# Kernel optimization log

Hardware: AMD Instinct MI355X
Metric: run time of the kernel (lower is better)

The kernel has to match this reference:

```python
import jax, jax.numpy as jnp
import numpy as np

F = 128          # gnn_out_features
D = 2 * F        # GNN_Emb width (mu || logvar)
N_SRC, N_DST = 50000, 10000
N_CATE, P = 18, 8
E = 100000
TAU = 1.0        # decay time constant (get_decay_weight assumed exp(-dt/tau))


def setup_inputs() -> dict:
    key = jax.random.key(0)
    ks = jax.random.split(key, 8)
    return {
        "gnn_emb_src": jax.random.normal(ks[0], (N_SRC, D), dtype=jnp.float32),
        "gnn_emb_dst": jax.random.normal(ks[1], (N_DST, D), dtype=jnp.float32),
        "news_pref": jax.random.normal(ks[2], (N_DST, N_CATE, P, D), dtype=jnp.float32),
        "last_update_time": jax.random.uniform(ks[3], (N_DST, N_CATE, P), dtype=jnp.float32),
        "time": jax.random.uniform(ks[4], (E,), dtype=jnp.float32),
        "cate_id": jax.random.randint(ks[5], (N_SRC,), 0, N_CATE),
        "src_idx": jax.random.randint(ks[6], (E,), 0, N_SRC),
        "dst_idx": jax.random.randint(ks[7], (E,), 0, N_DST),
    }


def reference(gnn_emb_src, gnn_emb_dst, news_pref, last_update_time,
              time, cate_id, src_idx, dst_idx):
    # --- per-edge gathers (DGL edges.src / edges.dst) ---
    src_emb = gnn_emb_src[src_idx, :F]                 # Representation, sample<=0  [E, F]
    cate = cate_id[src_idx]                            # [E]
    lut = last_update_time[dst_idx, cate]              # category-specific       [E, P]
    pref = news_pref[dst_idx, cate]                    # category-specific       [E, P, D]

    # --- decay-weighted fusion ---
    delta_t = time[0] - lut                            # Time[0] - Last_Update_Time [E, P]
    w = jnp.exp(-delta_t / TAU)                        # get_decay_weight         [E, P]
    target = gnn_emb_dst[dst_idx][:, None, :]          # dst GNN_Emb broadcast    [E, 1, D]
    decayed = pref * w[..., None] + target * (1.0 - w[..., None])  # [E, P, D]
    pref_emb = decayed[..., :F]                        # mu half, sample<=0       [E, P, F]

    # --- scaled dot-product attention: query=src_emb over P pref slots ---
    scores = jnp.einsum('ef,epf->ep', src_emb, pref_emb) / jnp.sqrt(jnp.float32(F))
    attn = jax.nn.softmax(scores, axis=-1)             # [E, P]
    dst_pref_emb = jnp.einsum('ep,epf->ef', attn, pref_emb)  # [E, F]

    # --- edge score ---
    return jnp.sum(src_emb * dst_pref_emb, axis=1)     # [E]
```

## Files before the change

### kernel.cpp

```cpp
#include <hip/hip_runtime.h>
#include <math.h>

#define F 128
#define D 256
#define N_CATE 18
#define P 8

__global__ __launch_bounds__(256) void score_predictor_kernel(
    const float* __restrict__ gnn_emb_src,
    const float* __restrict__ gnn_emb_dst,
    const float* __restrict__ news_pref,
    const float* __restrict__ last_update,
    const float* __restrict__ time_arr,
    const int*   __restrict__ cate_id,
    const int*   __restrict__ src_idx,
    const int*   __restrict__ dst_idx,
    float* __restrict__ out,
    int E)
{
    const int wave = (int)((blockIdx.x * blockDim.x + threadIdx.x) >> 6);
    const int lane = (int)(threadIdx.x & 63);
    if (wave >= E) return;
    const int e = wave;

    const int s = src_idx[e];
    const int d = dst_idx[e];
    const int c = cate_id[s];
    const float t0 = time_arr[0];

    const float* __restrict__ srow = gnn_emb_src + (size_t)s * D;
    const float* __restrict__ drow = gnn_emb_dst + (size_t)d * D;
    const size_t dc = (size_t)d * N_CATE + (size_t)c;
    const float* __restrict__ prow = news_pref + dc * (size_t)(P * D);
    const float* __restrict__ lrow = last_update + dc * (size_t)P;

    const float2 src2 = *(const float2*)(srow + 2 * lane);
    const float2 tgt2 = *(const float2*)(drow + 2 * lane);

    float w[P];
#pragma unroll
    for (int p = 0; p < P; ++p) {
        w[p] = __expf(lrow[p] - t0);
    }

    float2 pe[P];
    float sc[P];
#pragma unroll
    for (int p = 0; p < P; ++p) {
        const float2 pr = *(const float2*)(prow + p * D + 2 * lane);
        const float wp = w[p];
        const float omw = 1.0f - wp;
        pe[p].x = pr.x * wp + tgt2.x * omw;
        pe[p].y = pr.y * wp + tgt2.y * omw;
        sc[p] = src2.x * pe[p].x + src2.y * pe[p].y;
    }

#pragma unroll
    for (int m = 32; m >= 1; m >>= 1) {
#pragma unroll
        for (int p = 0; p < P; ++p) {
            sc[p] += __shfl_xor(sc[p], m, 64);
        }
    }

    const float inv_sqrtF = 0.088388347648318447f;
    float mx = -INFINITY;
#pragma unroll
    for (int p = 0; p < P; ++p) {
        sc[p] *= inv_sqrtF;
        mx = fmaxf(mx, sc[p]);
    }
    float sum = 0.0f;
    float a[P];
#pragma unroll
    for (int p = 0; p < P; ++p) {
        a[p] = __expf(sc[p] - mx);
        sum += a[p];
    }
    const float inv = 1.0f / sum;

    float2 dpe = make_float2(0.0f, 0.0f);
#pragma unroll
    for (int p = 0; p < P; ++p) {
        const float ap = a[p] * inv;
        dpe.x += ap * pe[p].x;
        dpe.y += ap * pe[p].y;
    }

    float part = src2.x * dpe.x + src2.y * dpe.y;
#pragma unroll
    for (int m = 32; m >= 1; m >>= 1) {
        part += __shfl_xor(part, m, 64);
    }
    if (lane == 0) {
        out[e] = part;
    }
}

extern "C" void kernel_launch(void* const* d_in, const int* in_sizes, int n_in,
                              void* d_out, int out_size, void* d_ws, size_t ws_size,
                              hipStream_t stream) {
    const float* gnn_emb_src = (const float*)d_in[0];
    const float* gnn_emb_dst = (const float*)d_in[1];
    const float* news_pref   = (const float*)d_in[2];
    const float* last_update = (const float*)d_in[3];
    const float* time_arr    = (const float*)d_in[4];
    const int*   cate_id     = (const int*)d_in[5];
    const int*   src_idx     = (const int*)d_in[6];
    const int*   dst_idx     = (const int*)d_in[7];
    float* out = (float*)d_out;

    const int E = in_sizes[6];
    const int waves_per_block = 256 / 64;
    const int grid = (E + waves_per_block - 1) / waves_per_block;

    score_predictor_kernel<<<grid, 256, 0, stream>>>(
        gnn_emb_src, gnn_emb_dst, news_pref, last_update, time_arr,
        cate_id, src_idx, dst_idx, out, E);
}
```

Measured before the change: 79.18 us.

## Compute edge score algebraically as attention-weighted scores, eight lanes per slot

Uses the identity that the final dot product equals sqrt(F) times the softmax-weighted mean of the per-slot scores, so the weighted pref vector is never materialised. Each group of 8 lanes handles one pref slot with float4 loads and computes src·pref and src·dst separately, combining them with the decay weight. This cuts shuffle reductions and per-lane registers. Rounding differs slightly from the original formulation.

```diff
diff --git a/kernel.cpp b/kernel.cpp
--- a/kernel.cpp
+++ b/kernel.cpp
@@ -22,6 +22,8 @@
     const int lane = (int)(threadIdx.x & 63);
     if (wave >= E) return;
     const int e = wave;
+    const int p = lane >> 3;
+    const int j = lane & 7;
 
     const int s = src_idx[e];
     const int d = dst_idx[e];
@@ -31,69 +33,48 @@
     const float* __restrict__ srow = gnn_emb_src + (size_t)s * D;
     const float* __restrict__ drow = gnn_emb_dst + (size_t)d * D;
     const size_t dc = (size_t)d * N_CATE + (size_t)c;
-    const float* __restrict__ prow = news_pref + dc * (size_t)(P * D);
-    const float* __restrict__ lrow = last_update + dc * (size_t)P;
+    const float* __restrict__ prow = news_pref + dc * (size_t)(P * D) + (size_t)p * D;
 
-    const float2 src2 = *(const float2*)(srow + 2 * lane);
-    const float2 tgt2 = *(const float2*)(drow + 2 * lane);
+    const float wp = __expf(last_update[dc * P + p] - t0);
+    const float omw = 1.0f - wp;
 
-    float w[P];
+    float qp = 0.0f, tp = 0.0f;
 #pragma unroll
-    for (int p = 0; p < P; ++p) {
-        w[p] = __expf(lrow[p] - t0);
-    }
-
-    float2 pe[P];
-    float sc[P];
-#pragma unroll
-    for (int p = 0; p < P; ++p) {
-        const float2 pr = *(const float2*)(prow + p * D + 2 * lane);
-        const float wp = w[p];
-        const float omw = 1.0f - wp;
-        pe[p].x = pr.x * wp + tgt2.x * omw;
-        pe[p].y = pr.y * wp + tgt2.y * omw;
-        sc[p] = src2.x * pe[p].x + src2.y * pe[p].y;
+    for (int k = 0; k < 4; ++k) {
+        const int off = k * 32 + j * 4;
+        const float4 sv = *(const float4*)(srow + off);
+        const float4 dv = *(const float4*)(drow + off);
+        const float4 pv = *(const float4*)(prow + off);
+        qp += sv.x * pv.x + sv.y * pv.y + sv.z * pv.z + sv.w * pv.w;
+        tp += sv.x * dv.x + sv.y * dv.y + sv.z * dv.z + sv.w * dv.w;
     }
 
 #pragma unroll
-    for (int m = 32; m >= 1; m >>= 1) {
-#pragma unroll
-        for (int p = 0; p < P; ++p) {
-            sc[p] += __shfl_xor(sc[p], m, 64);
-        }
+    for (int m = 1; m <= 4; m <<= 1) {
+        qp += __shfl_xor(qp, m, 64);
+        tp += __shfl_xor(tp, m, 64);
     }
 
     const float inv_sqrtF = 0.088388347648318447f;
-    float mx = -INFINITY;
+    const float sp = (wp * qp + omw * tp) * inv_sqrtF;
+
+    float mx = sp;
 #pragma unroll
-    for (int p = 0; p < P; ++p) {
-        sc[p] *= inv_sqrtF;
-        mx = fmaxf(mx, sc[p]);
-    }
-    float sum = 0.0f;
-    float a[P];
-#pragma unroll
-    for (int p = 0; p < P; ++p) {
-        a[p] = __expf(sc[p] - mx);
-        sum += a[p];
-    }
-    const float inv = 1.0f / sum;
-
-    float2 dpe = make_float2(0.0f, 0.0f);
-#pragma unroll
-    for (int p = 0; p < P; ++p) {
-        const float ap = a[p] * inv;
-        dpe.x += ap * pe[p].x;
-        dpe.y += ap * pe[p].y;
+    for (int m = 8; m <= 32; m <<= 1) {
+        mx = fmaxf(mx, __shfl_xor(mx, m, 64));
     }
 
-    float part = src2.x * dpe.x + src2.y * dpe.y;
+    const float ep = __expf(sp - mx);
+    float num = ep * sp;
+    float den = ep;
 #pragma unroll
-    for (int m = 32; m >= 1; m >>= 1) {
-        part += __shfl_xor(part, m, 64);
+    for (int m = 8; m <= 32; m <<= 1) {
+        num += __shfl_xor(num, m, 64);
+        den += __shfl_xor(den, m, 64);
     }
+
     if (lane == 0) {
-        out[e] = part;
+        out[e] = (num / den) * 11.313708498984761f;
     }
 }
 
```

After: 79.70 us. About the same (+0.7%).
